# Kernel tuning notes

Measured on AMD Instinct MI355X. Metric: run time of the kernel, lower is better.

The kernel has to match this reference:

```python
import jax, jax.numpy as jnp
import numpy as np

DIM = 512; HEADS = 8; DIM_HEAD = 64; DEPTH = 6; EMB = 512; NCLS = 1024; DIN = EMB + 12
ROT = 32; NBUCK = 8; MAXDIST = 32
SCALE = DIM_HEAD ** -0.5


def _bucket(rel):
    # T5-style causal relative position bucket (num_buckets=8, max_distance=32)
    n = jnp.maximum(-rel, 0)
    max_exact = NBUCK // 2
    is_small = n < max_exact
    vl = max_exact + (jnp.log(jnp.maximum(n, 1).astype(jnp.float32) / max_exact)
                      / np.log(MAXDIST / max_exact) * (NBUCK - max_exact)).astype(jnp.int32)
    vl = jnp.minimum(vl, NBUCK - 1)
    return jnp.where(is_small, n, vl)


def _scalenorm(x, g):
    n = jnp.linalg.norm(x, axis=-1, keepdims=True) * (DIM ** -0.5)
    return x / jnp.maximum(n, 1e-5) * g


def setup_inputs() -> dict:
    key = jax.random.key(0)
    ki = iter(jax.random.split(key, 24))
    B, S = 8, 1025
    cls = jax.random.randint(next(ki), (B, S, 1), 0, NCLS).astype(jnp.float32)
    vals = jax.random.uniform(next(ki), (B, S, 12), jnp.float32)
    saml = jnp.concatenate([cls, vals], -1)
    w = lambda *sh: jax.random.normal(next(ki), sh, jnp.float32) * 0.02
    return dict(
        saml=saml,
        emb_table=w(NCLS, EMB),
        proj_in_w=w(DIN, DIM), proj_in_b=jnp.zeros((DIM,), jnp.float32),
        g_attn=jnp.ones((DEPTH,), jnp.float32), g_ff=jnp.ones((DEPTH,), jnp.float32),
        Wq=w(DEPTH, DIM, DIM), Wk=w(DEPTH, DIM, DIM), Wv=w(DEPTH, DIM, DIM),
        Wo=w(DEPTH, DIM, DIM), bo=jnp.zeros((DEPTH, DIM), jnp.float32),
        relpos=w(NBUCK, HEADS),
        W1=w(DEPTH, DIM, 4 * DIM), b1=jnp.zeros((DEPTH, 4 * DIM), jnp.float32),
        W2=w(DEPTH, 4 * DIM, DIM), b2=jnp.zeros((DEPTH, DIM), jnp.float32),
        ln_g=jnp.ones((DIM,), jnp.float32), ln_b=jnp.zeros((DIM,), jnp.float32),
        proj_out_w=w(DIM, DIN), proj_out_b=jnp.zeros((DIN,), jnp.float32),
        cls_w=w(EMB, NCLS), cls_b=jnp.zeros((NCLS,), jnp.float32))


def reference(saml, emb_table, proj_in_w, proj_in_b, g_attn, g_ff, Wq, Wk, Wv, Wo, bo,
              relpos, W1, b1, W2, b2, ln_g, ln_b, proj_out_w, proj_out_b, cls_w, cls_b):
    x_in = saml[:, :-1]                                        # [B,S,13]
    idx = x_in[..., 0].astype(jnp.int32)
    x = jnp.concatenate([emb_table[idx], x_in[..., 1:]], -1)   # [B,S,DIN]
    h = x @ proj_in_w + proj_in_b                              # [B,S,DIM]
    B, S, _ = h.shape
    # rotary tables (rotary dim = 32, applied to first 32 dims of each head)
    inv = 1.0 / (10000.0 ** (jnp.arange(0, ROT, 2, dtype=jnp.float32) / ROT))
    pos = jnp.arange(S, dtype=jnp.float32)
    fr = pos[:, None] * inv[None, :]
    fr = jnp.concatenate([fr, fr], -1)                         # [S,ROT]
    cos, sin = jnp.cos(fr), jnp.sin(fr)

    def rot(v):  # v: [B,H,S,Dh]
        vl, vr = v[..., :ROT], v[..., ROT:]
        v1, v2 = vl[..., :ROT // 2], vl[..., ROT // 2:]
        return jnp.concatenate([vl * cos + jnp.concatenate([-v2, v1], -1) * sin, vr], -1)

    # relative position bucket bias (shared across layers), scaled by sqrt(dim_head)
    ip = jnp.arange(S)
    bucket = _bucket(ip[None, :] - ip[:, None])                # [S,S]
    bias = relpos[bucket].transpose(2, 0, 1) * (DIM_HEAD ** 0.5)  # [H,S,S]
    causal = jnp.tril(jnp.ones((S, S), bool))
    neg = -jnp.finfo(h.dtype).max
    split = lambda t: t.reshape(B, S, HEADS, DIM_HEAD).transpose(0, 2, 1, 3)

    for l in range(DEPTH):
        hn = _scalenorm(h, g_attn[l])
        q, k, v = split(hn @ Wq[l]), split(hn @ Wk[l]), split(hn @ Wv[l])
        q, k = rot(q), rot(k)
        dots = jnp.einsum('bhid,bhjd->bhij', q, k) * SCALE + bias
        attn = jax.nn.softmax(jnp.where(causal, dots, neg), axis=-1)
        o = jnp.einsum('bhij,bhjd->bhid', attn, v).transpose(0, 2, 1, 3).reshape(B, S, DIM)
        h = h + o @ Wo[l] + bo[l]
        hn = _scalenorm(h, g_ff[l])
        h = h + jax.nn.gelu(hn @ W1[l] + b1[l], approximate=False) @ W2[l] + b2[l]

    mu = h.mean(-1, keepdims=True)
    var = ((h - mu) ** 2).mean(-1, keepdims=True)
    h = (h - mu) / jnp.sqrt(var + 1e-5) * ln_g + ln_b
    out = h @ proj_out_w + proj_out_b                          # [B,S,DIN]
    emb_g = (out[..., :EMB] @ cls_w + cls_b).transpose(0, 2, 1)  # [B,NCLS,S]; NCLS == S
    return jnp.concatenate([emb_g, out[..., EMB:]], -1)        # [B,S,S+12]
```

## Files before the change

### kernel.cpp

```cpp
#include <hip/hip_runtime.h>
#include <math.h>

#define TOKENS 8192
#define SEQ    1024
#define BATCH  8
#define DIMM   512
#define NHEADS 8
#define DH     64
#define NDEPTH 6
#define HID    2048
#define NCLS_  1024
#define OUTC   1036
#define KPIN   544
#define LDK    72

typedef __attribute__((ext_vector_type(8))) short bf16x8;
typedef __attribute__((ext_vector_type(4))) float f32x4;

__device__ __forceinline__ float b2f(unsigned short u) {
    return __uint_as_float(((unsigned)u) << 16);
}
__device__ __forceinline__ unsigned short f2b(float f) {
    unsigned u = __float_as_uint(f);
    u += 0x7FFFu + ((u >> 16) & 1u);
    return (unsigned short)(u >> 16);
}
__device__ __forceinline__ void gl_lds16(const void* g, void* l) {
    __builtin_amdgcn_global_load_lds((const __attribute__((address_space(1))) void*)g,
                                     (__attribute__((address_space(3))) void*)l, 16, 0, 0);
}

template<int MODE>
__global__ __launch_bounds__(256) void gemm_bf16(
    const unsigned short* __restrict__ A, int Kp,
    const unsigned short* __restrict__ Bt,
    const float* __restrict__ bias,
    float* __restrict__ Cf,
    unsigned short* __restrict__ Cb,
    int N)
{
    __shared__ unsigned short As[128 * 32];
    __shared__ unsigned short Bs[128 * 32];
    const int tid = threadIdx.x;
    const int lane = tid & 63, wid = tid >> 6;
    const int wr = wid >> 1, wc = wid & 1;
    const int m0 = blockIdx.y * 128, n0 = blockIdx.x * 128;

    f32x4 acc[4][4] = {};

    const int srow = lane >> 2;
    const int skk  = (lane & 3) * 8;

    for (int k0 = 0; k0 < Kp; k0 += 32) {
        #pragma unroll
        for (int c = 0; c < 2; ++c) {
            int chunk = wid * 2 + c;
            int row = chunk * 16 + srow;
            gl_lds16(A  + (size_t)(m0 + row) * Kp + k0 + skk, As + chunk * 512);
            gl_lds16(Bt + (size_t)(n0 + row) * Kp + k0 + skk, Bs + chunk * 512);
        }
        __syncthreads();
        bf16x8 a[4], b[4];
        const int fr = lane & 15, fo = (lane >> 4) * 8;
        #pragma unroll
        for (int mi = 0; mi < 4; ++mi)
            a[mi] = *(const bf16x8*)(As + (wr * 64 + mi * 16 + fr) * 32 + fo);
        #pragma unroll
        for (int ni = 0; ni < 4; ++ni)
            b[ni] = *(const bf16x8*)(Bs + (wc * 64 + ni * 16 + fr) * 32 + fo);
        #pragma unroll
        for (int mi = 0; mi < 4; ++mi)
            #pragma unroll
            for (int ni = 0; ni < 4; ++ni)
                acc[mi][ni] = __builtin_amdgcn_mfma_f32_16x16x32_bf16(a[mi], b[ni], acc[mi][ni], 0, 0, 0);
        __syncthreads();
    }

    const int col16 = lane & 15;
    const int rbase = (lane >> 4) * 4;

    if (MODE == 7) {
        const int nbase = n0 + wc * 64;
        const int which = nbase >> 9;
        const int col0 = nbase & 511;
        unsigned short* dst = Cb + (size_t)which * ((size_t)TOKENS * DIMM);
        if (which < 2) {
            const float invp = powf(10000.0f, -(float)col16 * (1.0f / 16.0f));
            #pragma unroll
            for (int mi = 0; mi < 4; ++mi) {
                #pragma unroll
                for (int r = 0; r < 4; ++r) {
                    int mm = m0 + wr * 64 + mi * 16 + rbase + r;
                    int s = mm & (SEQ - 1);
                    float sn, cs;
                    sincosf((float)s * invp, &sn, &cs);
                    float v0 = acc[mi][0][r], v1 = acc[mi][1][r];
                    size_t base = (size_t)mm * DIMM + col0 + col16;
                    dst[base]      = f2b(v0 * cs - v1 * sn);
                    dst[base + 16] = f2b(v1 * cs + v0 * sn);
                    dst[base + 32] = f2b(acc[mi][2][r]);
                    dst[base + 48] = f2b(acc[mi][3][r]);
                }
            }
        } else {
            #pragma unroll
            for (int mi = 0; mi < 4; ++mi)
                #pragma unroll
                for (int ni = 0; ni < 4; ++ni)
                    #pragma unroll
                    for (int r = 0; r < 4; ++r) {
                        int mm = m0 + wr * 64 + mi * 16 + rbase + r;
                        dst[(size_t)mm * DIMM + col0 + ni * 16 + col16] = f2b(acc[mi][ni][r]);
                    }
        }
        return;
    }

    #pragma unroll
    for (int mi = 0; mi < 4; ++mi) {
        #pragma unroll
        for (int ni = 0; ni < 4; ++ni) {
            int nn = n0 + wc * 64 + ni * 16 + col16;
            if (MODE == 4 && nn >= 524) continue;
            float bv = (MODE == 1) ? 0.f : bias[nn];
            #pragma unroll
            for (int r = 0; r < 4; ++r) {
                int mm = m0 + wr * 64 + mi * 16 + rbase + r;
                float vv = acc[mi][ni][r] + bv;
                if (MODE == 3) vv = 0.5f * vv * (1.0f + erff(vv * 0.70710678118654752f));
                if (MODE == 0) Cf[(size_t)mm * N + nn] = vv;
                if (MODE == 1 || MODE == 3) Cb[(size_t)mm * N + nn] = f2b(vv);
                if (MODE == 2) Cf[(size_t)mm * N + nn] += vv;
                if (MODE == 4) {
                    if (nn < 512) Cb[(size_t)mm * 512 + nn] = f2b(vv);
                    else {
                        int bb = mm >> 10, ss = mm & 1023;
                        Cf[(size_t)bb * (SEQ * OUTC) + (size_t)ss * OUTC + 512 + nn] = vv;
                    }
                }
                if (MODE == 5) {
                    int bb = mm >> 10, ss = mm & 1023;
                    Cf[(size_t)bb * (NCLS_ * OUTC) + (size_t)nn * OUTC + ss] = vv;
                }
            }
        }
    }
}

__global__ __launch_bounds__(256) void convw_kernel(
    const float* __restrict__ src, unsigned short* __restrict__ dst,
    int K, int N, int Kp, long sstride, long dstride)
{
    src += (size_t)blockIdx.z * sstride;
    dst += (size_t)blockIdx.z * dstride;
    __shared__ float t[32][33];
    int k0 = blockIdx.y * 32, n0 = blockIdx.x * 32;
    int tx = threadIdx.x & 31, ty = threadIdx.x >> 5;
    #pragma unroll
    for (int i = 0; i < 4; ++i) {
        int k = k0 + ty + i * 8, n = n0 + tx;
        t[ty + i * 8][tx] = (k < K && n < N) ? src[(size_t)k * N + n] : 0.f;
    }
    __syncthreads();
    #pragma unroll
    for (int i = 0; i < 4; ++i) {
        int n = n0 + ty + i * 8;
        dst[(size_t)n * Kp + k0 + tx] = f2b(t[tx][ty + i * 8]);
    }
}

__global__ __launch_bounds__(256) void embed_kernel(
    const float* __restrict__ saml, const float* __restrict__ emb,
    unsigned short* __restrict__ x)
{
    int e = blockIdx.x * 256 + threadIdx.x;
    if (e >= TOKENS * KPIN) return;
    int t = e / KPIN, c = e % KPIN;
    int b = t >> 10, s = t & 1023;
    const float* row = saml + ((size_t)b * 1025 + s) * 13;
    float v;
    if (c < DIMM) v = emb[(size_t)((int)row[0]) * DIMM + c];
    else if (c < 524) v = row[1 + (c - DIMM)];
    else v = 0.f;
    x[(size_t)t * KPIN + c] = f2b(v);
}

__global__ __launch_bounds__(256) void scalenorm_kernel(
    const float* __restrict__ x, unsigned short* __restrict__ y,
    const float* __restrict__ gptr)
{
    int row = blockIdx.x;
    const float* xr = x + (size_t)row * DIMM;
    int tid = threadIdx.x, lane = tid & 63, wid = tid >> 6;
    float v0 = xr[tid], v1 = xr[tid + 256];
    float ss = v0 * v0 + v1 * v1;
    for (int off = 32; off; off >>= 1) ss += __shfl_down(ss, off, 64);
    __shared__ float red[4];
    if (lane == 0) red[wid] = ss;
    __syncthreads();
    float tot = red[0] + red[1] + red[2] + red[3];
    float n = sqrtf(tot) * 0.04419417382415922f;
    float f = gptr[0] / fmaxf(n, 1e-5f);
    y[(size_t)row * DIMM + tid]       = f2b(v0 * f);
    y[(size_t)row * DIMM + tid + 256] = f2b(v1 * f);
}

__global__ __launch_bounds__(256) void ln_kernel(
    const float* __restrict__ x, unsigned short* __restrict__ y,
    const float* __restrict__ g, const float* __restrict__ bb)
{
    int row = blockIdx.x;
    const float* xr = x + (size_t)row * DIMM;
    int tid = threadIdx.x, lane = tid & 63, wid = tid >> 6;
    float v0 = xr[tid], v1 = xr[tid + 256];
    __shared__ float red[4];
    float sum = v0 + v1;
    for (int off = 32; off; off >>= 1) sum += __shfl_down(sum, off, 64);
    if (lane == 0) red[wid] = sum;
    __syncthreads();
    float mu = (red[0] + red[1] + red[2] + red[3]) * (1.0f / 512.0f);
    __syncthreads();
    float d0 = v0 - mu, d1 = v1 - mu;
    float vs = d0 * d0 + d1 * d1;
    for (int off = 32; off; off >>= 1) vs += __shfl_down(vs, off, 64);
    if (lane == 0) red[wid] = vs;
    __syncthreads();
    float var = (red[0] + red[1] + red[2] + red[3]) * (1.0f / 512.0f);
    float inv = 1.0f / sqrtf(var + 1e-5f);
    y[(size_t)row * DIMM + tid]       = f2b(d0 * inv * g[tid] + bb[tid]);
    y[(size_t)row * DIMM + tid + 256] = f2b(d1 * inv * g[tid + 256] + bb[tid + 256]);
}

__global__ __launch_bounds__(256) void fattn_kernel(
    const unsigned short* __restrict__ q, const unsigned short* __restrict__ k,
    const unsigned short* __restrict__ v,
    const float* __restrict__ relpos, unsigned short* __restrict__ o)
{
    const int qt = blockIdx.x;
    const int h = blockIdx.y;
    const int b = blockIdx.z;
    const int tid = threadIdx.x;
    const int lane = tid & 63, wid = tid >> 6;
    const int l15 = lane & 15, hi = lane >> 4;

    __shared__ __align__(16) unsigned short Ks[64 * LDK];
    __shared__ __align__(16) unsigned short Vt[64 * LDK];
    __shared__ __align__(16) unsigned short Ps[64 * LDK];
    __shared__ float bias_d[SEQ];

    const size_t bh = (size_t)b * SEQ * DIMM + (size_t)h * DH;
    const int i0 = qt * 64;

    for (int n = tid; n < SEQ; n += 256) {
        int bucket;
        if (n < 4) bucket = n;
        else {
            int vl = 4 + (int)(logf((float)n * 0.25f) * (4.0f / logf(8.0f)));
            bucket = vl < 7 ? vl : 7;
        }
        bias_d[n] = relpos[bucket * NHEADS + h] * 8.0f;
    }

    bf16x8 qf[2];
    {
        const unsigned short* qrow = q + bh + (size_t)(i0 + wid * 16 + l15) * DIMM;
        qf[0] = *(const bf16x8*)(qrow + hi * 8);
        qf[1] = *(const bf16x8*)(qrow + 32 + hi * 8);
    }

    f32x4 o_acc[4] = {};
    float m_r[4], l_r[4];
    #pragma unroll
    for (int r = 0; r < 4; ++r) { m_r[r] = -3.0e38f; l_r[r] = 0.f; }

    for (int jt = 0; jt <= qt; ++jt) {
        const int j0 = jt * 64;
        __syncthreads();
        #pragma unroll
        for (int it = 0; it < 2; ++it) {
            int e = tid + 256 * it;
            int j = e >> 3;
            int d8 = (e & 7) * 8;
            uint4 kv = *(const uint4*)(k + bh + (size_t)(j0 + j) * DIMM + d8);
            *(uint4*)&Ks[j * LDK + d8] = kv;
            uint4 vv = *(const uint4*)(v + bh + (size_t)(j0 + j) * DIMM + d8);
            const unsigned short* p8 = (const unsigned short*)&vv;
            #pragma unroll
            for (int jj = 0; jj < 8; ++jj)
                Vt[(d8 + jj) * LDK + j] = p8[jj];
        }
        __syncthreads();

        f32x4 sacc[4] = {};
        #pragma unroll
        for (int nj = 0; nj < 4; ++nj) {
            #pragma unroll
            for (int kk = 0; kk < 2; ++kk) {
                bf16x8 kf = *(const bf16x8*)(Ks + (nj * 16 + l15) * LDK + kk * 32 + hi * 8);
                sacc[nj] = __builtin_amdgcn_mfma_f32_16x16x32_bf16(qf[kk], kf, sacc[nj], 0, 0, 0);
            }
        }

        float s4[4][4];
        const bool diag = (jt == qt);
        const int gi_base = i0 + wid * 16 + hi * 4;
        #pragma unroll
        for (int nj = 0; nj < 4; ++nj) {
            int gj = j0 + nj * 16 + l15;
            #pragma unroll
            for (int r = 0; r < 4; ++r) {
                int gi = gi_base + r;
                if (diag && gj > gi) s4[nj][r] = -1.0e30f;
                else s4[nj][r] = sacc[nj][r] * 0.125f + bias_d[gi - gj];
            }
        }

        float rm[4];
        #pragma unroll
        for (int r = 0; r < 4; ++r)
            rm[r] = fmaxf(fmaxf(s4[0][r], s4[1][r]), fmaxf(s4[2][r], s4[3][r]));
        #pragma unroll
        for (int off = 1; off < 16; off <<= 1)
            #pragma unroll
            for (int r = 0; r < 4; ++r)
                rm[r] = fmaxf(rm[r], __shfl_xor(rm[r], off, 64));

        float pscale[4];
        #pragma unroll
        for (int r = 0; r < 4; ++r) {
            float mn = fmaxf(m_r[r], rm[r]);
            pscale[r] = __expf(m_r[r] - mn);
            m_r[r] = mn;
        }
        float rs[4] = {};
        #pragma unroll
        for (int nj = 0; nj < 4; ++nj)
            #pragma unroll
            for (int r = 0; r < 4; ++r) {
                float e = __expf(s4[nj][r] - m_r[r]);
                rs[r] += e;
                Ps[(wid * 16 + hi * 4 + r) * LDK + nj * 16 + l15] = f2b(e);
            }
        #pragma unroll
        for (int off = 1; off < 16; off <<= 1)
            #pragma unroll
            for (int r = 0; r < 4; ++r)
                rs[r] += __shfl_xor(rs[r], off, 64);
        #pragma unroll
        for (int r = 0; r < 4; ++r)
            l_r[r] = l_r[r] * pscale[r] + rs[r];
        #pragma unroll
        for (int ni = 0; ni < 4; ++ni)
            #pragma unroll
            for (int r = 0; r < 4; ++r)
                o_acc[ni][r] *= pscale[r];
        __syncthreads();

        #pragma unroll
        for (int kk = 0; kk < 2; ++kk) {
            bf16x8 pf = *(const bf16x8*)(Ps + (wid * 16 + l15) * LDK + kk * 32 + hi * 8);
            #pragma unroll
            for (int ni = 0; ni < 4; ++ni) {
                bf16x8 vf = *(const bf16x8*)(Vt + (ni * 16 + l15) * LDK + kk * 32 + hi * 8);
                o_acc[ni] = __builtin_amdgcn_mfma_f32_16x16x32_bf16(pf, vf, o_acc[ni], 0, 0, 0);
            }
        }
    }

    #pragma unroll
    for (int r = 0; r < 4; ++r) {
        float inv = 1.0f / l_r[r];
        int gi = i0 + wid * 16 + hi * 4 + r;
        #pragma unroll
        for (int ni = 0; ni < 4; ++ni)
            o[bh + (size_t)gi * DIMM + ni * 16 + l15] = f2b(o_acc[ni][r] * inv);
    }
}

extern "C" void kernel_launch(void* const* d_in, const int* in_sizes, int n_in,
                              void* d_out, int out_size, void* d_ws, size_t ws_size,
                              hipStream_t stream)
{
    const float* saml       = (const float*)d_in[0];
    const float* emb_table  = (const float*)d_in[1];
    const float* proj_in_w  = (const float*)d_in[2];
    const float* proj_in_b  = (const float*)d_in[3];
    const float* g_attn     = (const float*)d_in[4];
    const float* g_ff       = (const float*)d_in[5];
    const float* Wq         = (const float*)d_in[6];
    const float* Wk         = (const float*)d_in[7];
    const float* Wv         = (const float*)d_in[8];
    const float* Wo         = (const float*)d_in[9];
    const float* bo         = (const float*)d_in[10];
    const float* relpos     = (const float*)d_in[11];
    const float* W1         = (const float*)d_in[12];
    const float* b1         = (const float*)d_in[13];
    const float* W2         = (const float*)d_in[14];
    const float* b2         = (const float*)d_in[15];
    const float* ln_g       = (const float*)d_in[16];
    const float* ln_b       = (const float*)d_in[17];
    const float* proj_out_w = (const float*)d_in[18];
    const float* proj_out_b = (const float*)d_in[19];
    const float* cls_w      = (const float*)d_in[20];
    const float* cls_b      = (const float*)d_in[21];
    float* out = (float*)d_out;

    char* wsp = (char*)d_ws;
    size_t woff = 0;
    auto carve = [&](size_t bytes) -> char* {
        char* p = wsp + woff;
        woff += (bytes + 255) & ~(size_t)255;
        return p;
    };
    typedef unsigned short u16;
    float* h  = (float*)carve((size_t)TOKENS * DIMM * 4);
    u16* qb   = (u16*)carve((size_t)TOKENS * DIMM * 2);
    u16* kb   = (u16*)carve((size_t)TOKENS * DIMM * 2);
    u16* vb   = (u16*)carve((size_t)TOKENS * DIMM * 2);
    u16* ab   = (u16*)carve((size_t)TOKENS * DIMM * 2);
    u16* ob   = (u16*)carve((size_t)TOKENS * DIMM * 2);
    u16* ff   = (u16*)carve((size_t)TOKENS * HID * 2);
    u16* ci   = (u16*)carve((size_t)TOKENS * DIMM * 2);
    u16* xb   = (u16*)carve((size_t)TOKENS * KPIN * 2);
    u16* qkvT = (u16*)carve((size_t)NDEPTH * 1536 * DIMM * 2);
    u16* woT  = (u16*)carve((size_t)NDEPTH * DIMM * DIMM * 2);
    u16* w1T  = (u16*)carve((size_t)NDEPTH * HID * DIMM * 2);
    u16* w2T  = (u16*)carve((size_t)NDEPTH * DIMM * HID * 2);
    u16* pinT = (u16*)carve((size_t)DIMM * KPIN * 2);
    u16* poutT= (u16*)carve((size_t)640 * DIMM * 2);
    u16* clsT = (u16*)carve((size_t)NCLS_ * DIMM * 2);

    dim3 blk(256);

    convw_kernel<<<dim3(16, 16, 6), blk, 0, stream>>>(Wq, qkvT,             512, 512, 512, 512*512, 1536*512);
    convw_kernel<<<dim3(16, 16, 6), blk, 0, stream>>>(Wk, qkvT + 512*512,   512, 512, 512, 512*512, 1536*512);
    convw_kernel<<<dim3(16, 16, 6), blk, 0, stream>>>(Wv, qkvT + 1024*512,  512, 512, 512, 512*512, 1536*512);
    convw_kernel<<<dim3(16, 16, 6), blk, 0, stream>>>(Wo, woT, 512, 512, 512, 512*512, 512*512);
    convw_kernel<<<dim3(64, 16, 6), blk, 0, stream>>>(W1, w1T, 512, 2048, 512, 512*2048, 2048*512);
    convw_kernel<<<dim3(16, 64, 6), blk, 0, stream>>>(W2, w2T, 2048, 512, 2048, 2048*512, 512*2048);
    convw_kernel<<<dim3(16, 17, 1), blk, 0, stream>>>(proj_in_w, pinT, 524, 512, KPIN, 0, 0);
    convw_kernel<<<dim3(20, 16, 1), blk, 0, stream>>>(proj_out_w, poutT, 512, 524, 512, 0, 0);
    convw_kernel<<<dim3(32, 16, 1), blk, 0, stream>>>(cls_w, clsT, 512, 1024, 512, 0, 0);

    embed_kernel<<<(TOKENS * KPIN + 255) / 256, blk, 0, stream>>>(saml, emb_table, xb);
    gemm_bf16<0><<<dim3(4, 64), blk, 0, stream>>>(xb, KPIN, pinT, proj_in_b, h, nullptr, DIMM);

    for (int l = 0; l < NDEPTH; ++l) {
        const u16* wqkv = qkvT + (size_t)l * 1536 * DIMM;
        const u16* wo = woT + (size_t)l * DIMM * DIMM;
        const u16* w1 = w1T + (size_t)l * HID * DIMM;
        const u16* w2 = w2T + (size_t)l * DIMM * HID;

        scalenorm_kernel<<<TOKENS, blk, 0, stream>>>(h, ab, g_attn + l);
        gemm_bf16<7><<<dim3(12, 64), blk, 0, stream>>>(ab, DIMM, wqkv, nullptr, nullptr, qb, DIMM);
        fattn_kernel<<<dim3(SEQ / 64, NHEADS, BATCH), blk, 0, stream>>>(qb, kb, vb, relpos, ob);
        gemm_bf16<2><<<dim3(4, 64), blk, 0, stream>>>(ob, DIMM, wo, bo + (size_t)l * DIMM, h, nullptr, DIMM);
        scalenorm_kernel<<<TOKENS, blk, 0, stream>>>(h, ab, g_ff + l);
        gemm_bf16<3><<<dim3(16, 64), blk, 0, stream>>>(ab, DIMM, w1, b1 + (size_t)l * HID, nullptr, ff, HID);
        gemm_bf16<2><<<dim3(4, 64), blk, 0, stream>>>(ff, HID, w2, b2 + (size_t)l * DIMM, h, nullptr, DIMM);
    }

    ln_kernel<<<TOKENS, blk, 0, stream>>>(h, ab, ln_g, ln_b);
    gemm_bf16<4><<<dim3(5, 64), blk, 0, stream>>>(ab, DIMM, poutT, proj_out_b, out, ci, 524);
    gemm_bf16<5><<<dim3(8, 64), blk, 0, stream>>>(ci, DIMM, clsT, cls_b, out, nullptr, NCLS_);
}
```

Baseline: 1.909 ms.

## Store V transposed from QKV GEMM, enlarge attention tiles, vectorize norm kernels

The QKV GEMM epilogue now writes V pre-transposed per (batch, head) so attention can copy K and V tiles into swizzled LDS with direct global-to-LDS loads instead of a scalar transpose. The attention kernel processes 128 query rows per block, pairs short and long causal tiles to balance work, skips fully masked per-wave tiles, and drops one barrier per iteration. Scalenorm and layernorm now give each row to one wavefront with vectorized loads and shuffle-only reductions. The risks are more registers per thread in attention, fewer blocks, and 8-byte strided stores in the GEMM epilogue.

After: 1.696 ms. 11.1% less time.

```diff
diff --git a/kernel.cpp b/kernel.cpp
--- a/kernel.cpp
+++ b/kernel.cpp
@@ -12,7 +12,6 @@
 #define NCLS_  1024
 #define OUTC   1036
 #define KPIN   544
-#define LDK    72
 
 typedef __attribute__((ext_vector_type(8))) short bf16x8;
 typedef __attribute__((ext_vector_type(4))) float f32x4;
@@ -83,8 +82,8 @@
         const int nbase = n0 + wc * 64;
         const int which = nbase >> 9;
         const int col0 = nbase & 511;
-        unsigned short* dst = Cb + (size_t)which * ((size_t)TOKENS * DIMM);
         if (which < 2) {
+            unsigned short* dst = Cb + (size_t)which * ((size_t)TOKENS * DIMM);
             const float invp = powf(10000.0f, -(float)col16 * (1.0f / 16.0f));
             #pragma unroll
             for (int mi = 0; mi < 4; ++mi) {
@@ -103,15 +102,21 @@
                 }
             }
         } else {
-            #pragma unroll
-            for (int mi = 0; mi < 4; ++mi)
-                #pragma unroll
-                for (int ni = 0; ni < 4; ++ni)
-                    #pragma unroll
-                    for (int r = 0; r < 4; ++r) {
-                        int mm = m0 + wr * 64 + mi * 16 + rbase + r;
-                        dst[(size_t)mm * DIMM + col0 + ni * 16 + col16] = f2b(acc[mi][ni][r]);
-                    }
+            unsigned short* vtb = Cb + (size_t)2 * TOKENS * DIMM;
+            #pragma unroll
+            for (int mi = 0; mi < 4; ++mi) {
+                int mm = m0 + wr * 64 + mi * 16 + rbase;
+                int bb = mm >> 10, ss = mm & 1023;
+                #pragma unroll
+                for (int ni = 0; ni < 4; ++ni) {
+                    int d_full = col0 + ni * 16 + col16;
+                    unsigned short t4[4];
+                    #pragma unroll
+                    for (int r = 0; r < 4; ++r) t4[r] = f2b(acc[mi][ni][r]);
+                    size_t idx = ((size_t)(bb * NHEADS + (d_full >> 6)) * DH + (d_full & 63)) * SEQ + ss;
+                    *(uint2*)(vtb + idx) = *(uint2*)t4;
+                }
+            }
         }
         return;
     }
@@ -189,67 +194,74 @@
     const float* __restrict__ x, unsigned short* __restrict__ y,
     const float* __restrict__ gptr)
 {
-    int row = blockIdx.x;
-    const float* xr = x + (size_t)row * DIMM;
-    int tid = threadIdx.x, lane = tid & 63, wid = tid >> 6;
-    float v0 = xr[tid], v1 = xr[tid + 256];
-    float ss = v0 * v0 + v1 * v1;
-    for (int off = 32; off; off >>= 1) ss += __shfl_down(ss, off, 64);
-    __shared__ float red[4];
-    if (lane == 0) red[wid] = ss;
-    __syncthreads();
-    float tot = red[0] + red[1] + red[2] + red[3];
-    float n = sqrtf(tot) * 0.04419417382415922f;
+    int row = blockIdx.x * 4 + (threadIdx.x >> 6);
+    int lane = threadIdx.x & 63;
+    const float* xr = x + (size_t)row * DIMM + lane * 8;
+    float4 a = *(const float4*)xr;
+    float4 c = *(const float4*)(xr + 4);
+    float ss = a.x*a.x + a.y*a.y + a.z*a.z + a.w*a.w
+             + c.x*c.x + c.y*c.y + c.z*c.z + c.w*c.w;
+    #pragma unroll
+    for (int off = 1; off < 64; off <<= 1) ss += __shfl_xor(ss, off, 64);
+    float n = sqrtf(ss) * 0.04419417382415922f;
     float f = gptr[0] / fmaxf(n, 1e-5f);
-    y[(size_t)row * DIMM + tid]       = f2b(v0 * f);
-    y[(size_t)row * DIMM + tid + 256] = f2b(v1 * f);
+    unsigned short t8[8] = { f2b(a.x*f), f2b(a.y*f), f2b(a.z*f), f2b(a.w*f),
+                             f2b(c.x*f), f2b(c.y*f), f2b(c.z*f), f2b(c.w*f) };
+    *(uint4*)(y + (size_t)row * DIMM + lane * 8) = *(uint4*)t8;
 }
 
 __global__ __launch_bounds__(256) void ln_kernel(
     const float* __restrict__ x, unsigned short* __restrict__ y,
     const float* __restrict__ g, const float* __restrict__ bb)
 {
-    int row = blockIdx.x;
-    const float* xr = x + (size_t)row * DIMM;
-    int tid = threadIdx.x, lane = tid & 63, wid = tid >> 6;
-    float v0 = xr[tid], v1 = xr[tid + 256];
-    __shared__ float red[4];
-    float sum = v0 + v1;
-    for (int off = 32; off; off >>= 1) sum += __shfl_down(sum, off, 64);
-    if (lane == 0) red[wid] = sum;
-    __syncthreads();
-    float mu = (red[0] + red[1] + red[2] + red[3]) * (1.0f / 512.0f);
-    __syncthreads();
-    float d0 = v0 - mu, d1 = v1 - mu;
-    float vs = d0 * d0 + d1 * d1;
-    for (int off = 32; off; off >>= 1) vs += __shfl_down(vs, off, 64);
-    if (lane == 0) red[wid] = vs;
-    __syncthreads();
-    float var = (red[0] + red[1] + red[2] + red[3]) * (1.0f / 512.0f);
-    float inv = 1.0f / sqrtf(var + 1e-5f);
-    y[(size_t)row * DIMM + tid]       = f2b(d0 * inv * g[tid] + bb[tid]);
-    y[(size_t)row * DIMM + tid + 256] = f2b(d1 * inv * g[tid + 256] + bb[tid + 256]);
+    int row = blockIdx.x * 4 + (threadIdx.x >> 6);
+    int lane = threadIdx.x & 63;
+    const float* xr = x + (size_t)row * DIMM + lane * 8;
+    float v[8];
+    *(float4*)&v[0] = *(const float4*)xr;
+    *(float4*)&v[4] = *(const float4*)(xr + 4);
+    float sum = 0.f;
+    #pragma unroll
+    for (int j = 0; j < 8; ++j) sum += v[j];
+    #pragma unroll
+    for (int off = 1; off < 64; off <<= 1) sum += __shfl_xor(sum, off, 64);
+    float mu = sum * (1.0f / 512.0f);
+    float vs = 0.f;
+    #pragma unroll
+    for (int j = 0; j < 8; ++j) { v[j] -= mu; vs += v[j] * v[j]; }
+    #pragma unroll
+    for (int off = 1; off < 64; off <<= 1) vs += __shfl_xor(vs, off, 64);
+    float inv = 1.0f / sqrtf(vs * (1.0f / 512.0f) + 1e-5f);
+    float4 g0 = *(const float4*)(g + lane * 8), g1 = *(const float4*)(g + lane * 8 + 4);
+    float4 b0 = *(const float4*)(bb + lane * 8), b1 = *(const float4*)(bb + lane * 8 + 4);
+    float gg[8] = {g0.x,g0.y,g0.z,g0.w,g1.x,g1.y,g1.z,g1.w};
+    float bv[8] = {b0.x,b0.y,b0.z,b0.w,b1.x,b1.y,b1.z,b1.w};
+    unsigned short t8[8];
+    #pragma unroll
+    for (int j = 0; j < 8; ++j) t8[j] = f2b(v[j] * inv * gg[j] + bv[j]);
+    *(uint4*)(y + (size_t)row * DIMM + lane * 8) = *(uint4*)t8;
 }
 
 __global__ __launch_bounds__(256) void fattn_kernel(
     const unsigned short* __restrict__ q, const unsigned short* __restrict__ k,
-    const unsigned short* __restrict__ v,
+    const unsigned short* __restrict__ vt,
     const float* __restrict__ relpos, unsigned short* __restrict__ o)
 {
-    const int qt = blockIdx.x;
-    const int h = blockIdx.y;
-    const int b = blockIdx.z;
+    const int bx = blockIdx.x;
+    const int qt = (bx & 1) ? (7 - (bx >> 1)) : (bx >> 1);
+    const int h = blockIdx.y, b = blockIdx.z;
     const int tid = threadIdx.x;
     const int lane = tid & 63, wid = tid >> 6;
     const int l15 = lane & 15, hi = lane >> 4;
 
-    __shared__ __align__(16) unsigned short Ks[64 * LDK];
-    __shared__ __align__(16) unsigned short Vt[64 * LDK];
-    __shared__ __align__(16) unsigned short Ps[64 * LDK];
+    __shared__ __align__(16) unsigned short Ks[64 * 64];
+    __shared__ __align__(16) unsigned short Vs[64 * 64];
+    __shared__ __align__(16) unsigned short Ps[128 * 64];
     __shared__ float bias_d[SEQ];
 
     const size_t bh = (size_t)b * SEQ * DIMM + (size_t)h * DH;
-    const int i0 = qt * 64;
+    const unsigned short* vtg = vt + (size_t)(b * NHEADS + h) * DH * SEQ;
+    const int i0 = qt * 128;
 
     for (int n = tid; n < SEQ; n += 256) {
         int bucket;
@@ -261,120 +273,139 @@
         bias_d[n] = relpos[bucket * NHEADS + h] * 8.0f;
     }
 
-    bf16x8 qf[2];
-    {
-        const unsigned short* qrow = q + bh + (size_t)(i0 + wid * 16 + l15) * DIMM;
-        qf[0] = *(const bf16x8*)(qrow + hi * 8);
-        qf[1] = *(const bf16x8*)(qrow + 32 + hi * 8);
-    }
-
-    f32x4 o_acc[4] = {};
-    float m_r[4], l_r[4];
-    #pragma unroll
-    for (int r = 0; r < 4; ++r) { m_r[r] = -3.0e38f; l_r[r] = 0.f; }
-
-    for (int jt = 0; jt <= qt; ++jt) {
+    bf16x8 qf[2][2];
+    #pragma unroll
+    for (int mi = 0; mi < 2; ++mi) {
+        const unsigned short* qrow = q + bh + (size_t)(i0 + wid * 32 + mi * 16 + l15) * DIMM;
+        qf[mi][0] = *(const bf16x8*)(qrow + hi * 8);
+        qf[mi][1] = *(const bf16x8*)(qrow + 32 + hi * 8);
+    }
+
+    f32x4 o_acc[2][4] = {};
+    float m_r[2][4], l_r[2][4];
+    #pragma unroll
+    for (int mi = 0; mi < 2; ++mi)
+        #pragma unroll
+        for (int r = 0; r < 4; ++r) { m_r[mi][r] = -3.0e38f; l_r[mi][r] = 0.f; }
+
+    const int s_lo = i0 + wid * 32;
+    const int jtmax = 2 * qt + 1;
+
+    const int swz = l15 & 7;
+
+    for (int jt = 0; jt <= jtmax; ++jt) {
         const int j0 = jt * 64;
         __syncthreads();
         #pragma unroll
         for (int it = 0; it < 2; ++it) {
-            int e = tid + 256 * it;
-            int j = e >> 3;
-            int d8 = (e & 7) * 8;
-            uint4 kv = *(const uint4*)(k + bh + (size_t)(j0 + j) * DIMM + d8);
-            *(uint4*)&Ks[j * LDK + d8] = kv;
-            uint4 vv = *(const uint4*)(v + bh + (size_t)(j0 + j) * DIMM + d8);
-            const unsigned short* p8 = (const unsigned short*)&vv;
-            #pragma unroll
-            for (int jj = 0; jj < 8; ++jj)
-                Vt[(d8 + jj) * LDK + j] = p8[jj];
+            int ci = (wid * 2 + it) * 64 + lane;
+            int j = ci >> 3, cp = ci & 7;
+            int cs = cp ^ (j & 7);
+            gl_lds16(k + bh + (size_t)(j0 + j) * DIMM + cs * 8,
+                     Ks + (size_t)(wid * 2 + it) * 512);
+            gl_lds16(vtg + (size_t)j * SEQ + j0 + cs * 8,
+                     Vs + (size_t)(wid * 2 + it) * 512);
         }
         __syncthreads();
 
-        f32x4 sacc[4] = {};
-        #pragma unroll
-        for (int nj = 0; nj < 4; ++nj) {
+        if (j0 <= s_lo + 31) {
+            f32x4 sacc[2][4] = {};
+            #pragma unroll
+            for (int nj = 0; nj < 4; ++nj) {
+                int row = nj * 16 + l15;
+                #pragma unroll
+                for (int kk = 0; kk < 2; ++kk) {
+                    bf16x8 kf = *(const bf16x8*)(Ks + row * 64 + (((4 * kk + hi) ^ swz) << 3));
+                    sacc[0][nj] = __builtin_amdgcn_mfma_f32_16x16x32_bf16(qf[0][kk], kf, sacc[0][nj], 0, 0, 0);
+                    sacc[1][nj] = __builtin_amdgcn_mfma_f32_16x16x32_bf16(qf[1][kk], kf, sacc[1][nj], 0, 0, 0);
+                }
+            }
+
+            const bool full = (j0 + 63 <= s_lo);
+            #pragma unroll
+            for (int mi = 0; mi < 2; ++mi) {
+                float s4[4][4];
+                #pragma unroll
+                for (int nj = 0; nj < 4; ++nj) {
+                    int gj = j0 + nj * 16 + l15;
+                    #pragma unroll
+                    for (int r = 0; r < 4; ++r) {
+                        int gi = s_lo + mi * 16 + hi * 4 + r;
+                        int d = gi - gj;
+                        float bd = bias_d[d < 0 ? 0 : d];
+                        float sv = sacc[mi][nj][r] * 0.125f + bd;
+                        s4[nj][r] = (!full && gj > gi) ? -3.0e38f : sv;
+                    }
+                }
+                float rm[4];
+                #pragma unroll
+                for (int r = 0; r < 4; ++r)
+                    rm[r] = fmaxf(fmaxf(s4[0][r], s4[1][r]), fmaxf(s4[2][r], s4[3][r]));
+                #pragma unroll
+                for (int off = 1; off < 16; off <<= 1)
+                    #pragma unroll
+                    for (int r = 0; r < 4; ++r)
+                        rm[r] = fmaxf(rm[r], __shfl_xor(rm[r], off, 64));
+                float pscale[4], rs[4] = {};
+                #pragma unroll
+                for (int r = 0; r < 4; ++r) {
+                    float mn = fmaxf(m_r[mi][r], rm[r]);
+                    pscale[r] = __expf(m_r[mi][r] - mn);
+                    m_r[mi][r] = mn;
+                }
+                #pragma unroll
+                for (int nj = 0; nj < 4; ++nj) {
+                    int chunk = 2 * nj + (l15 >> 3);
+                    #pragma unroll
+                    for (int r = 0; r < 4; ++r) {
+                        float e = __expf(s4[nj][r] - m_r[mi][r]);
+                        rs[r] += e;
+                        int i_loc = wid * 32 + mi * 16 + hi * 4 + r;
+                        Ps[i_loc * 64 + ((chunk ^ (i_loc & 7)) << 3) + (l15 & 7)] = f2b(e);
+                    }
+                }
+                #pragma unroll
+                for (int off = 1; off < 16; off <<= 1)
+                    #pragma unroll
+                    for (int r = 0; r < 4; ++r)
+                        rs[r] += __shfl_xor(rs[r], off, 64);
+                #pragma unroll
+                for (int r = 0; r < 4; ++r)
+                    l_r[mi][r] = l_r[mi][r] * pscale[r] + rs[r];
+                #pragma unroll
+                for (int ni = 0; ni < 4; ++ni)
+                    #pragma unroll
+                    for (int r = 0; r < 4; ++r)
+                        o_acc[mi][ni][r] *= pscale[r];
+            }
+
             #pragma unroll
             for (int kk = 0; kk < 2; ++kk) {
-                bf16x8 kf = *(const bf16x8*)(Ks + (nj * 16 + l15) * LDK + kk * 32 + hi * 8);
-                sacc[nj] = __builtin_amdgcn_mfma_f32_16x16x32_bf16(qf[kk], kf, sacc[nj], 0, 0, 0);
-            }
-        }
-
-        float s4[4][4];
-        const bool diag = (jt == qt);
-        const int gi_base = i0 + wid * 16 + hi * 4;
-        #pragma unroll
-        for (int nj = 0; nj < 4; ++nj) {
-            int gj = j0 + nj * 16 + l15;
-            #pragma unroll
-            for (int r = 0; r < 4; ++r) {
-                int gi = gi_base + r;
-                if (diag && gj > gi) s4[nj][r] = -1.0e30f;
-                else s4[nj][r] = sacc[nj][r] * 0.125f + bias_d[gi - gj];
-            }
-        }
-
-        float rm[4];
-        #pragma unroll
-        for (int r = 0; r < 4; ++r)
-            rm[r] = fmaxf(fmaxf(s4[0][r], s4[1][r]), fmaxf(s4[2][r], s4[3][r]));
-        #pragma unroll
-        for (int off = 1; off < 16; off <<= 1)
-            #pragma unroll
-            for (int r = 0; r < 4; ++r)
-                rm[r] = fmaxf(rm[r], __shfl_xor(rm[r], off, 64));
-
-        float pscale[4];
+                int rp0 = wid * 32 + l15;
+                int rp1 = wid * 32 + 16 + l15;
+                bf16x8 pf0 = *(const bf16x8*)(Ps + rp0 * 64 + (((4 * kk + hi) ^ (rp0 & 7)) << 3));
+                bf16x8 pf1 = *(const bf16x8*)(Ps + rp1 * 64 + (((4 * kk + hi) ^ (rp1 & 7)) << 3));
+                #pragma unroll
+                for (int ni = 0; ni < 4; ++ni) {
+                    int rv = ni * 16 + l15;
+                    bf16x8 vf = *(const bf16x8*)(Vs + rv * 64 + (((4 * kk + hi) ^ swz) << 3));
+                    o_acc[0][ni] = __builtin_amdgcn_mfma_f32_16x16x32_bf16(pf0, vf, o_acc[0][ni], 0, 0, 0);
+                    o_acc[1][ni] = __builtin_amdgcn_mfma_f32_16x16x32_bf16(pf1, vf, o_acc[1][ni], 0, 0, 0);
+                }
+            }
+        }
+    }
+
+    #pragma unroll
+    for (int mi = 0; mi < 2; ++mi)
         #pragma unroll
         for (int r = 0; r < 4; ++r) {
-            float mn = fmaxf(m_r[r], rm[r]);
-            pscale[r] = __expf(m_r[r] - mn);
-            m_r[r] = mn;
-        }
-        float rs[4] = {};
-        #pragma unroll
-        for (int nj = 0; nj < 4; ++nj)
-            #pragma unroll
-            for (int r = 0; r < 4; ++r) {
-                float e = __expf(s4[nj][r] - m_r[r]);
-                rs[r] += e;
-                Ps[(wid * 16 + hi * 4 + r) * LDK + nj * 16 + l15] = f2b(e);
-            }
-        #pragma unroll
-        for (int off = 1; off < 16; off <<= 1)
-            #pragma unroll
-            for (int r = 0; r < 4; ++r)
-                rs[r] += __shfl_xor(rs[r], off, 64);
-        #pragma unroll
-        for (int r = 0; r < 4; ++r)
-            l_r[r] = l_r[r] * pscale[r] + rs[r];
-        #pragma unroll
-        for (int ni = 0; ni < 4; ++ni)
-            #pragma unroll
-            for (int r = 0; r < 4; ++r)
-                o_acc[ni][r] *= pscale[r];
-        __syncthreads();
-
-        #pragma unroll
-        for (int kk = 0; kk < 2; ++kk) {
-            bf16x8 pf = *(const bf16x8*)(Ps + (wid * 16 + l15) * LDK + kk * 32 + hi * 8);
-            #pragma unroll
-            for (int ni = 0; ni < 4; ++ni) {
-                bf16x8 vf = *(const bf16x8*)(Vt + (ni * 16 + l15) * LDK + kk * 32 + hi * 8);
-                o_acc[ni] = __builtin_amdgcn_mfma_f32_16x16x32_bf16(pf, vf, o_acc[ni], 0, 0, 0);
-            }
-        }
-    }
-
-    #pragma unroll
-    for (int r = 0; r < 4; ++r) {
-        float inv = 1.0f / l_r[r];
-        int gi = i0 + wid * 16 + hi * 4 + r;
-        #pragma unroll
-        for (int ni = 0; ni < 4; ++ni)
-            o[bh + (size_t)gi * DIMM + ni * 16 + l15] = f2b(o_acc[ni][r] * inv);
-    }
+            float inv = 1.0f / l_r[mi][r];
+            int gi = i0 + wid * 32 + mi * 16 + hi * 4 + r;
+            #pragma unroll
+            for (int ni = 0; ni < 4; ++ni)
+                o[bh + (size_t)gi * DIMM + ni * 16 + l15] = f2b(o_acc[mi][ni][r] * inv);
+        }
 }
 
 extern "C" void kernel_launch(void* const* d_in, const int* in_sizes, int n_in,
@@ -414,9 +445,9 @@
     };
     typedef unsigned short u16;
     float* h  = (float*)carve((size_t)TOKENS * DIMM * 4);
-    u16* qb   = (u16*)carve((size_t)TOKENS * DIMM * 2);
-    u16* kb   = (u16*)carve((size_t)TOKENS * DIMM * 2);
-    u16* vb   = (u16*)carve((size_t)TOKENS * DIMM * 2);
+    u16* qb   = (u16*)carve((size_t)TOKENS * DIMM * 2 * 3);
+    u16* kb   = qb + (size_t)TOKENS * DIMM;
+    u16* vtb  = kb + (size_t)TOKENS * DIMM;
     u16* ab   = (u16*)carve((size_t)TOKENS * DIMM * 2);
     u16* ob   = (u16*)carve((size_t)TOKENS * DIMM * 2);
     u16* ff   = (u16*)carve((size_t)TOKENS * HID * 2);
@@ -451,16 +482,16 @@
         const u16* w1 = w1T + (size_t)l * HID * DIMM;
         const u16* w2 = w2T + (size_t)l * DIMM * HID;
 
-        scalenorm_kernel<<<TOKENS, blk, 0, stream>>>(h, ab, g_attn + l);
+        scalenorm_kernel<<<TOKENS / 4, blk, 0, stream>>>(h, ab, g_attn + l);
         gemm_bf16<7><<<dim3(12, 64), blk, 0, stream>>>(ab, DIMM, wqkv, nullptr, nullptr, qb, DIMM);
-        fattn_kernel<<<dim3(SEQ / 64, NHEADS, BATCH), blk, 0, stream>>>(qb, kb, vb, relpos, ob);
+        fattn_kernel<<<dim3(8, NHEADS, BATCH), blk, 0, stream>>>(qb, kb, vtb, relpos, ob);
         gemm_bf16<2><<<dim3(4, 64), blk, 0, stream>>>(ob, DIMM, wo, bo + (size_t)l * DIMM, h, nullptr, DIMM);
-        scalenorm_kernel<<<TOKENS, blk, 0, stream>>>(h, ab, g_ff + l);
+        scalenorm_kernel<<<TOKENS / 4, blk, 0, stream>>>(h, ab, g_ff + l);
         gemm_bf16<3><<<dim3(16, 64), blk, 0, stream>>>(ab, DIMM, w1, b1 + (size_t)l * HID, nullptr, ff, HID);
         gemm_bf16<2><<<dim3(4, 64), blk, 0, stream>>>(ff, HID, w2, b2 + (size_t)l * DIMM, h, nullptr, DIMM);
     }
 
-    ln_kernel<<<TOKENS, blk, 0, stream>>>(h, ab, ln_g, ln_b);
+    ln_kernel<<<TOKENS / 4, blk, 0, stream>>>(h, ab, ln_g, ln_b);
     gemm_bf16<4><<<dim3(5, 64), blk, 0, stream>>>(ab, DIMM, poutT, proj_out_b, out, ci, 524);
     gemm_bf16<5><<<dim3(8, 64), blk, 0, stream>>>(ci, DIMM, clsT, cls_b, out, nullptr, NCLS_);
 }
```
